# Optimization experiments

Hardware: AMD Instinct MI355X
Metric: run time of the kernel (lower is better)

Reference implementation:

```python
import jax, jax.numpy as jnp
import numpy as np

B, S, D, H, DH, M = 4, 4096, 1024, 16, 64, 128


def _create_projection_matrix(m, d, seed=0):
    # Block-orthogonal Gaussian projection (FAVOR+), same math as the numpy helper.
    np.random.seed(seed)
    n_block = m // d
    blocks = []
    for _ in range(n_block):
        block = np.random.normal(0, 1, (d, d))
        q, _ = np.linalg.qr(block)
        blocks.append(q.T)
    rem = m - n_block * d
    if rem > 0:
        block = np.random.normal(0, 1, (d, d))
        q, _ = np.linalg.qr(block)
        blocks.append(q.T[:rem])
    proj = np.vstack(blocks)
    multiplier = np.linalg.norm(np.random.normal(0, 1, (m, d)), axis=1)
    return (np.diag(multiplier) @ proj).astype(np.float32)


def setup_inputs() -> dict:
    key = jax.random.key(0)
    ks = jax.random.split(key, 8)
    lim_attn = np.sqrt(6.0 / (D + H * DH)).astype(np.float32)
    lim_out = np.sqrt(6.0 / (H * DH + D)).astype(np.float32)
    head_pos = np.linspace(0.0 + 1.0 / (2.0 * H), 1.0, H, endpoint=False, dtype=np.float32).reshape(1, 1, H, 1)
    return {
        "source_input": jax.random.normal(ks[0], (B, S, D), jnp.float32),
        "pos_ft": jax.random.normal(ks[1], (B, S, D), jnp.float32),
        "pos_ft_slopes": jax.random.normal(ks[2], (B, S, D), jnp.float32),
        "value_weight": jax.random.uniform(ks[3], (D, H, DH), jnp.float32, -lim_attn, lim_attn),
        "pos_ft_weight": jax.random.uniform(ks[4], (D, H, DH), jnp.float32, -lim_attn, lim_attn),
        "pos_ft_scale": jnp.ones((1, 1, H, 1), jnp.float32),
        "pos_ft_offsets": jnp.asarray(head_pos),
        "output_weight": jax.random.uniform(ks[5], (H * DH, D), jnp.float32, -lim_out, lim_out),
        "projection_matrix": jnp.asarray(_create_projection_matrix(M, DH, seed=1234)),
    }


def _fourier_features(x, projection_matrix):
    # x: [b, l, h, d] -> [b, l, h, 2m]
    d = x.shape[-1]
    m = projection_matrix.shape[0]
    data_normalizer = 1.0 / (float(d) ** 0.25)
    ratio = 1.0 / (float(m) ** 0.5)
    xd = jnp.einsum('blhd,md->blhm', data_normalizer * x, projection_matrix)
    xd = jnp.clip(xd, -10000.0, 10000.0)
    return jnp.concatenate([ratio * jnp.sin(xd), ratio * jnp.cos(xd)], axis=-1)


def reference(source_input, pos_ft, pos_ft_slopes, value_weight, pos_ft_weight,
              pos_ft_scale, pos_ft_offsets, output_weight, projection_matrix):
    # Projections
    value = jnp.einsum('bnm,mhd->bnhd', source_input, value_weight)        # [B,S,H,DH]
    pos_proj = jnp.einsum('bnm,mhd->bnhd', pos_ft, pos_ft_weight)          # [B,S,H,DH]
    slope_proj = jnp.einsum('bnm,mhd->bnhd', pos_ft_slopes, pos_ft_weight) # [B,S,H,DH]

    query_pos = pos_ft_scale * pos_proj
    key_pos = query_pos + pos_ft_offsets * (pos_ft_scale * slope_proj)

    # FAVOR fourier random features
    q_prime = _fourier_features(query_pos, projection_matrix)  # [B,S,H,2M]
    k_prime = _fourier_features(key_pos, projection_matrix)    # [B,S,H,2M]

    # Linear attention: O(L) kvs accumulation (non-causal, normalize_attn=False)
    kvs = jnp.einsum('blhm,blhd->bhmd', k_prime, value)         # [B,H,2M,DH]
    av = jnp.einsum('blhm,bhmd->blhd', q_prime, kvs)            # [B,S,H,DH]

    slen = av.shape[1]
    norms = jnp.linalg.norm(slope_proj, axis=-1, keepdims=True) / float(slen)
    av = norms * av

    out = jnp.einsum('bnm,md->bnd', av.reshape(av.shape[0], slen, -1), output_weight)
    # Dropout is identity at inference (training=False)
    return out
```

## Files before the change

### kernel.cpp

```cpp
#include <hip/hip_runtime.h>
#include <math.h>


typedef unsigned short u16;
typedef __attribute__((ext_vector_type(8))) short bf16x8;
typedef __attribute__((ext_vector_type(4))) float floatx4;

__device__ __forceinline__ float bf2f(u16 u) {
  union { unsigned int i; float f; } v; v.i = ((unsigned int)u) << 16; return v.f;
}
__device__ __forceinline__ u16 f2bf(float f) {
  union { float f; unsigned int i; } v; v.f = f;
  unsigned int r = v.i + 0x7fffu + ((v.i >> 16) & 1u);
  return (u16)(r >> 16);
}
__device__ __forceinline__ bool wire_f32(const unsigned* probe) {
  return probe[0] == 0x3F800000u;
}
__device__ __forceinline__ void gload_lds16(const void* g, void* l) {
  __builtin_amdgcn_global_load_lds(
      (const __attribute__((address_space(1))) void*)g,
      (__attribute__((address_space(3))) void*)l, 16, 0, 0);
}

__device__ __forceinline__ void gemm_body(
    const u16* __restrict__ A, int lda, const u16* __restrict__ B, int ldb,
    void* __restrict__ C, long coff, int Klog, int fold, int ofmt, bool f32w,
    long m0, long n0, u16* sA, u16* sB)
{
  const int t = threadIdx.x;
  const int wave = t >> 6, lane = t & 63;
  const int ll = lane & 15, quad = lane >> 4;
  const int wm0 = (wave >> 1) * 64, wn0 = (wave & 1) * 64;
  const int lr = lane >> 2, lc = (lane & 3) * 8;
  floatx4 acc[4][4];
  floatx4 zero = {0.0f, 0.0f, 0.0f, 0.0f};
  #pragma unroll
  for (int i = 0; i < 4; i++)
    #pragma unroll
    for (int j = 0; j < 4; j++) acc[i][j] = zero;

  for (int kc = 0; kc < Klog; kc += 32) {
    int akc = kc, bkc = kc;
    if (fold) {
      akc = (kc < 1024) ? kc : kc - 1024;
      bkc = (kc < 2048) ? kc : kc - 2048;
    }
    #pragma unroll
    for (int j = 0; j < 2; j++) {
      int r0 = wave * 32 + j * 16;
      gload_lds16(&A[(m0 + r0 + lr) * (long)lda + akc + lc], &sA[r0 * 32]);
      gload_lds16(&B[(n0 + r0 + lr) * (long)ldb + bkc + lc], &sB[r0 * 32]);
    }
    __syncthreads();
    bf16x8 af[4], bfr[4];
    #pragma unroll
    for (int i = 0; i < 4; i++) {
      af[i]  = *(const bf16x8*)&sA[(wm0 + i * 16 + ll) * 32 + quad * 8];
      bfr[i] = *(const bf16x8*)&sB[(wn0 + i * 16 + ll) * 32 + quad * 8];
    }
    #pragma unroll
    for (int i = 0; i < 4; i++)
      #pragma unroll
      for (int j = 0; j < 4; j++)
        acc[i][j] = __builtin_amdgcn_mfma_f32_16x16x32_bf16(af[i], bfr[j], acc[i][j], 0, 0, 0);
    __syncthreads();
  }
  #pragma unroll
  for (int i = 0; i < 4; i++)
    #pragma unroll
    for (int j = 0; j < 4; j++)
      #pragma unroll
      for (int r = 0; r < 4; r++) {
        long row = m0 + wm0 + i * 16 + quad * 4 + r;
        long col = n0 + wn0 + j * 16 + ll;
        float v = acc[i][j][r];
        long addr = coff + row * 1024 + col;
        if (ofmt == 0) ((u16*)C)[addr] = f2bf(v);
        else if (ofmt == 1) ((float*)C)[addr] = v;
        else if (f32w) ((float*)C)[addr] = v;
        else ((u16*)C)[addr] = f2bf(v);
      }
}

__global__ __launch_bounds__(256) void gemm_gl(
    const u16* __restrict__ A, int lda, const u16* __restrict__ B, int ldb,
    void* __restrict__ C, long coff, int Klog, int fold, int ofmt,
    const unsigned* __restrict__ probe)
{
  __shared__ u16 sA[128 * 32], sB[128 * 32];
  gemm_body(A, lda, B, ldb, C, coff, Klog, fold, ofmt, wire_f32(probe),
            (long)blockIdx.x * 128, (long)blockIdx.y * 128, sA, sB);
}

__global__ __launch_bounds__(256) void gemm_mega(
    const u16* __restrict__ A2, const u16* __restrict__ W2,
    float* __restrict__ posp, const u16* __restrict__ srcb,
    const u16* __restrict__ wvt, u16* __restrict__ valb,
    const unsigned* __restrict__ probe)
{
  __shared__ u16 sA[128 * 32], sB[128 * 32];
  const bool f32w = wire_f32(probe);
  int id = blockIdx.x;
  if (id < 512) {
    gemm_body(A2, 2048, W2, 2048, posp, 0, 3072, 1, 1, f32w,
              (long)(id >> 3) * 128, (long)(id & 7) * 128, sA, sB);
  } else {
    int v = id - 512;
    gemm_body(srcb, 1024, wvt, 1024, valb, 0, 1024, 0, 0, f32w,
              (long)(v >> 3) * 128, (long)(v & 7) * 128, sA, sB);
  }
}

__device__ __forceinline__ void split_body(
    const void* __restrict__ Aw, long aoff, u16* __restrict__ A2, int rowbase,
    bool f32w, long idx)
{
  int row = (int)(idx >> 7);
  int c8 = (int)(idx & 127) * 8;
  u16 h8[8], l8[8];
  if (f32w) {
    const float* ap = (const float*)Aw + aoff + (long)row * 1024 + c8;
    #pragma unroll
    for (int e = 0; e < 8; e++) {
      float v = ap[e]; u16 hb = f2bf(v);
      h8[e] = hb; l8[e] = f2bf(v - bf2f(hb));
    }
  } else {
    *(uint4*)h8 = *(const uint4*)((const u16*)Aw + aoff + (long)row * 1024 + c8);
    #pragma unroll
    for (int e = 0; e < 8; e++) l8[e] = 0;
  }
  u16* orow = A2 + (long)(rowbase + row) * 2048;
  *(uint4*)&orow[c8] = *(uint4*)h8;
  *(uint4*)&orow[1024 + c8] = *(uint4*)l8;
}

__device__ __forceinline__ void conv_body(
    const void* __restrict__ Aw, long aoff, u16* __restrict__ out,
    bool f32w, long idx)
{
  long base = idx * 8;
  u16 h8[8];
  if (f32w) {
    const float* ap = (const float*)Aw + aoff + base;
    #pragma unroll
    for (int e = 0; e < 8; e++) h8[e] = f2bf(ap[e]);
  } else {
    *(uint4*)h8 = *(const uint4*)((const u16*)Aw + aoff + base);
  }
  *(uint4*)&out[base] = *(uint4*)h8;
}

__global__ __launch_bounds__(256) void split_hilo(
    const void* __restrict__ Aw, long aoff, u16* __restrict__ A2, int rowbase,
    const unsigned* __restrict__ probe)
{
  split_body(Aw, aoff, A2, rowbase, wire_f32(probe),
             (long)blockIdx.x * 256 + threadIdx.x);
}

__global__ __launch_bounds__(256) void conv_bf16(
    const void* __restrict__ Aw, long aoff, u16* __restrict__ out,
    const unsigned* __restrict__ probe)
{
  conv_body(Aw, aoff, out, wire_f32(probe),
            (long)blockIdx.x * 256 + threadIdx.x);
}

__global__ __launch_bounds__(256) void mega2(
    const u16* __restrict__ av, const u16* __restrict__ wot,
    void* __restrict__ dout, long coff,
    const void* __restrict__ posf, const void* __restrict__ slpf,
    const void* __restrict__ src, long ioff_next,
    u16* __restrict__ A2, u16* __restrict__ srcb,
    const unsigned* __restrict__ probe)
{
  __shared__ u16 sA[128 * 32], sB[128 * 32];
  const bool f32w = wire_f32(probe);
  int id = blockIdx.x;
  if (id < 256) {
    gemm_body(av, 1024, wot, 1024, dout, coff, 1024, 0, 2, f32w,
              (long)(id >> 3) * 128, (long)(id & 7) * 128, sA, sB);
  } else if (id < 2304) {
    split_body(posf, ioff_next, A2, 0, f32w,
               (long)(id - 256) * 256 + threadIdx.x);
  } else if (id < 4352) {
    split_body(slpf, ioff_next, A2, 4096, f32w,
               (long)(id - 2304) * 256 + threadIdx.x);
  } else {
    conv_body(src, ioff_next, srcb, f32w,
              (long)(id - 4352) * 256 + threadIdx.x);
  }
}

__global__ __launch_bounds__(256) void transpose_w(
    const void* __restrict__ in, u16* __restrict__ outb,
    const unsigned* __restrict__ probe)
{
  __shared__ float s[64][65];
  const bool f32w = wire_f32(probe);
  int t = threadIdx.x;
  int r0 = blockIdx.y * 64, c0 = blockIdx.x * 64;
  for (int u = t; u < 4096; u += 256) {
    int r = u >> 6, c = u & 63;
    long idx = (long)(r0 + r) * 1024 + c0 + c;
    s[c][r] = f32w ? ((const float*)in)[idx] : bf2f(((const u16*)in)[idx]);
  }
  __syncthreads();
  for (int u = t; u < 4096; u += 256) {
    int r = u >> 6, c = u & 63;
    outb[(long)(c0 + r) * 1024 + r0 + c] = f2bf(s[r][c]);
  }
}

__global__ __launch_bounds__(256) void transpose_w2(
    const void* __restrict__ in, u16* __restrict__ out2,
    const unsigned* __restrict__ probe)
{
  __shared__ float s[64][65];
  const bool f32w = wire_f32(probe);
  int t = threadIdx.x;
  int r0 = blockIdx.y * 64, c0 = blockIdx.x * 64;
  for (int u = t; u < 4096; u += 256) {
    int r = u >> 6, c = u & 63;
    long idx = (long)(r0 + r) * 1024 + c0 + c;
    s[c][r] = f32w ? ((const float*)in)[idx] : bf2f(((const u16*)in)[idx]);
  }
  __syncthreads();
  for (int u = t; u < 4096; u += 256) {
    int r = u >> 6, c = u & 63;
    float v = s[r][c];
    u16 hb = f2bf(v);
    long rowb = (long)(c0 + r) * 2048;
    out2[rowb + r0 + c] = hb;
    out2[rowb + 1024 + r0 + c] = f2bf(v - bf2f(hb));
  }
}

__global__ __launch_bounds__(256) void proj_prep(
    const void* __restrict__ proj, u16* __restrict__ P2,
    const unsigned* __restrict__ probe)
{
  const bool f32w = wire_f32(probe);
  int idx = blockIdx.x * 256 + threadIdx.x;
  int m = idx >> 6, d = idx & 63;
  const float dn = 0.3535533905932738f;
  float v = dn * (f32w ? ((const float*)proj)[idx] : bf2f(((const u16*)proj)[idx]));
  u16 hb = f2bf(v);
  P2[(long)m * 128 + d] = hb;
  P2[(long)m * 128 + 64 + d] = f2bf(v - bf2f(hb));
}

__global__ __launch_bounds__(256) void featurize_mfma(
    const float* __restrict__ posp, const float* __restrict__ slpp,
    const u16* __restrict__ P2, const void* __restrict__ scl,
    const void* __restrict__ offs, u16* __restrict__ qp, u16* __restrict__ kpT,
    const unsigned* __restrict__ probe, int h0)
{
  __shared__ u16 sAp[4 * 64 * 32], sAs[4 * 64 * 32], sB[4 * 128 * 32];
  const bool f32w = wire_f32(probe);
  const int t = threadIdx.x;
  const int wave = t >> 6, lane = t & 63;
  const int ll = lane & 15, quad = lane >> 4;
  const int wm0 = (wave >> 1) * 32, wn0 = (wave & 1) * 64;
  const int g = blockIdx.y, h = h0 + g;
  const int l0 = blockIdx.x * 64;
  const float s1 = f32w ? ((const float*)scl)[h] : bf2f(((const u16*)scl)[h]);
  const float s2 = (f32w ? ((const float*)offs)[h] : bf2f(((const u16*)offs)[h])) * s1;
  const float ratio = 0.08838834764831845f;

  for (int u = t; u < 512; u += 256) {
    int r = u >> 3, cc = u & 7;
    const float* pp = posp + (long)(l0 + r) * 1024 + h * 64 + cc * 8;
    const float* sp = slpp + (long)(l0 + r) * 1024 + h * 64 + cc * 8;
    u16 ph[8], pl[8], sh[8], sl[8];
    #pragma unroll
    for (int e = 0; e < 8; e++) {
      float vp = pp[e]; u16 hb = f2bf(vp);
      ph[e] = hb; pl[e] = f2bf(vp - bf2f(hb));
      float vs = sp[e]; u16 sb = f2bf(vs);
      sh[e] = sb; sl[e] = f2bf(vs - bf2f(sb));
    }
    int ch = cc >> 2, cw = (cc & 3) * 8;
    *(uint4*)&sAp[((ch) * 64 + r) * 32 + cw]     = *(uint4*)ph;
    *(uint4*)&sAp[((2 + ch) * 64 + r) * 32 + cw] = *(uint4*)pl;
    *(uint4*)&sAs[((ch) * 64 + r) * 32 + cw]     = *(uint4*)sh;
    *(uint4*)&sAs[((2 + ch) * 64 + r) * 32 + cw] = *(uint4*)sl;
  }
  for (int u = t; u < 2048; u += 256) {
    int r = u >> 4, q4 = u & 15;
    uint4 v = *(const uint4*)&P2[(long)r * 128 + q4 * 8];
    int ch = q4 >> 2, cw = (q4 & 3) * 8;
    *(uint4*)&sB[(ch * 128 + r) * 32 + cw] = v;
  }
  __syncthreads();

  floatx4 accp[2][4], accs[2][4];
  floatx4 zero = {0.0f, 0.0f, 0.0f, 0.0f};
  #pragma unroll
  for (int i = 0; i < 2; i++)
    #pragma unroll
    for (int j = 0; j < 4; j++) { accp[i][j] = zero; accs[i][j] = zero; }

  const int ACH[6] = {0, 1, 0, 1, 2, 3};
  const int BCH[6] = {0, 1, 2, 3, 0, 1};
  #pragma unroll
  for (int kci = 0; kci < 6; kci++) {
    int ac = ACH[kci], bc = BCH[kci];
    bf16x8 ap[2], as2[2], bfr[4];
    #pragma unroll
    for (int i = 0; i < 2; i++) {
      ap[i]  = *(const bf16x8*)&sAp[(ac * 64 + wm0 + i * 16 + ll) * 32 + quad * 8];
      as2[i] = *(const bf16x8*)&sAs[(ac * 64 + wm0 + i * 16 + ll) * 32 + quad * 8];
    }
    #pragma unroll
    for (int j = 0; j < 4; j++)
      bfr[j] = *(const bf16x8*)&sB[(bc * 128 + wn0 + j * 16 + ll) * 32 + quad * 8];
    #pragma unroll
    for (int i = 0; i < 2; i++)
      #pragma unroll
      for (int j = 0; j < 4; j++) {
        accp[i][j] = __builtin_amdgcn_mfma_f32_16x16x32_bf16(ap[i],  bfr[j], accp[i][j], 0, 0, 0);
        accs[i][j] = __builtin_amdgcn_mfma_f32_16x16x32_bf16(as2[i], bfr[j], accs[i][j], 0, 0, 0);
      }
  }

  #pragma unroll
  for (int i = 0; i < 2; i++) {
    int lbase = l0 + wm0 + i * 16 + quad * 4;
    #pragma unroll
    for (int j = 0; j < 4; j++) {
      int m = wn0 + j * 16 + ll;
      u16 ksin[4], kcos[4];
      #pragma unroll
      for (int r = 0; r < 4; r++) {
        float dq = s1 * accp[i][j][r];
        float dk = dq + s2 * accs[i][j][r];
        dq = fminf(fmaxf(dq, -10000.0f), 10000.0f);
        dk = fminf(fmaxf(dk, -10000.0f), 10000.0f);
        long qbase = ((long)g * 4096 + lbase + r) * 256;
        qp[qbase + m]       = f2bf(ratio * __sinf(dq));
        qp[qbase + m + 128] = f2bf(ratio * __cosf(dq));
        ksin[r] = f2bf(ratio * __sinf(dk));
        kcos[r] = f2bf(ratio * __cosf(dk));
      }
      *(uint2*)&kpT[((long)(g * 256 + m)) * 4096 + lbase]       = *(uint2*)ksin;
      *(uint2*)&kpT[((long)(g * 256 + m + 128)) * 4096 + lbase] = *(uint2*)kcos;
    }
  }
}

__global__ __launch_bounds__(256) void transpose_v(
    const u16* __restrict__ in, u16* __restrict__ out)
{
  __shared__ u16 s[64][72];
  int t = threadIdx.x;
  int c0 = blockIdx.x * 64;
  int r0 = blockIdx.y * 64;
  for (int u = t; u < 512; u += 256) {
    int r = u >> 3, c8 = (u & 7) * 8;
    uint4 v = *(const uint4*)&in[(long)(r0 + r) * 1024 + c0 + c8];
    const u16* pv = (const u16*)&v;
    #pragma unroll
    for (int e = 0; e < 8; e++) s[c8 + e][r] = pv[e];
  }
  __syncthreads();
  for (int u = t; u < 512; u += 256) {
    int r = u >> 3, c8 = (u & 7) * 8;
    *(uint4*)&out[(long)(c0 + r) * 4096 + r0 + c8] = *(const uint4*)&s[r][c8];
  }
}

__global__ __launch_bounds__(256) void norm_kernel(
    const float* __restrict__ slp, float* __restrict__ nrm)
{
  int idx = blockIdx.x * 256 + threadIdx.x;
  int row = idx >> 4, h = idx & 15;
  const float* p = slp + (long)row * 1024 + h * 64;
  float acc = 0.0f;
  #pragma unroll
  for (int i = 0; i < 16; i++) {
    float4 v = *(const float4*)&p[i * 4];
    acc += v.x * v.x + v.y * v.y + v.z * v.z + v.w * v.w;
  }
  nrm[idx] = sqrtf(acc) * (1.0f / 4096.0f);
}

__global__ __launch_bounds__(256) void kvs_mfma(
    const u16* __restrict__ kpT, const u16* __restrict__ vT,
    float* __restrict__ kvp, int h0)
{
  __shared__ u16 sA[256][40], sB[64][40];
  const int t = threadIdx.x;
  const int wave = t >> 6, lane = t & 63;
  const int ll = lane & 15, quad = lane >> 4;
  const int wm0 = wave * 64;
  const int ks = blockIdx.x, g = blockIdx.y;
  const int G = gridDim.y, KS = gridDim.x;
  const int h = h0 + g;
  const int lch = 4096 / KS;
  const int lbase = ks * lch;
  floatx4 acc[4][4];
  floatx4 zero = {0.0f, 0.0f, 0.0f, 0.0f};
  #pragma unroll
  for (int i = 0; i < 4; i++)
    #pragma unroll
    for (int j = 0; j < 4; j++) acc[i][j] = zero;

  for (int kc = 0; kc < lch; kc += 32) {
    for (int u = t; u < 1024; u += 256) {
      int r = u >> 2, s = u & 3;
      *(uint4*)&sA[r][s * 8] =
          *(const uint4*)&kpT[((long)(g * 256 + r)) * 4096 + lbase + kc + s * 8];
    }
    {
      int r = t >> 2, s = t & 3;
      if (t < 256)
        *(uint4*)&sB[r][s * 8] =
            *(const uint4*)&vT[((long)(h * 64 + r)) * 4096 + lbase + kc + s * 8];
    }
    __syncthreads();
    bf16x8 af[4], bfr[4];
    #pragma unroll
    for (int i = 0; i < 4; i++) {
      af[i] = *(const bf16x8*)&sA[wm0 + i * 16 + ll][quad * 8];
      bfr[i] = *(const bf16x8*)&sB[i * 16 + ll][quad * 8];
    }
    #pragma unroll
    for (int i = 0; i < 4; i++)
      #pragma unroll
      for (int j = 0; j < 4; j++)
        acc[i][j] = __builtin_amdgcn_mfma_f32_16x16x32_bf16(af[i], bfr[j], acc[i][j], 0, 0, 0);
    __syncthreads();
  }
  long obase = ((long)ks * G + g) * 256;
  #pragma unroll
  for (int i = 0; i < 4; i++)
    #pragma unroll
    for (int j = 0; j < 4; j++)
      #pragma unroll
      for (int r = 0; r < 4; r++) {
        int row = wm0 + i * 16 + quad * 4 + r;
        int col = j * 16 + ll;
        kvp[(obase + row) * 64 + col] = acc[i][j][r];
      }
}

__global__ __launch_bounds__(256) void kvs_reduce(
    const float* __restrict__ kvp, u16* __restrict__ kvsTh,
    u16* __restrict__ kvsTl, int G, int KS)
{
  int idx = blockIdx.x * 256 + threadIdx.x;
  int m = idx & 255, d = (idx >> 8) & 63, g = idx >> 14;
  float s = 0.0f;
  for (int p = 0; p < KS; p++)
    s += kvp[(((long)p * G + g) * 256 + m) * 64 + d];
  u16 hb = f2bf(s);
  long o = ((long)g * 64 + d) * 256 + m;
  kvsTh[o] = hb;
  kvsTl[o] = f2bf(s - bf2f(hb));
}

__global__ __launch_bounds__(256) void av_mfma(
    const u16* __restrict__ qp, const u16* __restrict__ kvsTh,
    const u16* __restrict__ kvsTl, const float* __restrict__ nrm,
    u16* __restrict__ av, int h0)
{
  __shared__ u16 sA[128][40], sBh[64][40], sBl[64][40];
  const int t = threadIdx.x;
  const int wave = t >> 6, lane = t & 63;
  const int ll = lane & 15, quad = lane >> 4;
  const int wm0 = wave * 32;
  const int g = blockIdx.y, h = h0 + g;
  const int l0 = blockIdx.x * 128;
  floatx4 acc[2][4];
  floatx4 zero = {0.0f, 0.0f, 0.0f, 0.0f};
  #pragma unroll
  for (int i = 0; i < 2; i++)
    #pragma unroll
    for (int j = 0; j < 4; j++) acc[i][j] = zero;

  for (int kc = 0; kc < 256; kc += 32) {
    for (int u = t; u < 512; u += 256) {
      int r = u >> 2, s = u & 3;
      *(uint4*)&sA[r][s * 8] =
          *(const uint4*)&qp[((long)g * 4096 + l0 + r) * 256 + kc + s * 8];
    }
    {
      int r = t >> 2, s4 = t & 3;
      long o = ((long)g * 64 + r) * 256 + kc + s4 * 8;
      *(uint4*)&sBh[r][s4 * 8] = *(const uint4*)&kvsTh[o];
      *(uint4*)&sBl[r][s4 * 8] = *(const uint4*)&kvsTl[o];
    }
    __syncthreads();
    bf16x8 af[2], bh[4], bl[4];
    #pragma unroll
    for (int i = 0; i < 2; i++)
      af[i] = *(const bf16x8*)&sA[wm0 + i * 16 + ll][quad * 8];
    #pragma unroll
    for (int j = 0; j < 4; j++) {
      bh[j] = *(const bf16x8*)&sBh[j * 16 + ll][quad * 8];
      bl[j] = *(const bf16x8*)&sBl[j * 16 + ll][quad * 8];
    }
    #pragma unroll
    for (int i = 0; i < 2; i++)
      #pragma unroll
      for (int j = 0; j < 4; j++) {
        acc[i][j] = __builtin_amdgcn_mfma_f32_16x16x32_bf16(af[i], bh[j], acc[i][j], 0, 0, 0);
        acc[i][j] = __builtin_amdgcn_mfma_f32_16x16x32_bf16(af[i], bl[j], acc[i][j], 0, 0, 0);
      }
    __syncthreads();
  }
  #pragma unroll
  for (int i = 0; i < 2; i++)
    #pragma unroll
    for (int r = 0; r < 4; r++) {
      int l = l0 + wm0 + i * 16 + quad * 4 + r;
      float nv = nrm[l * 16 + h];
      #pragma unroll
      for (int j = 0; j < 4; j++) {
        int d = j * 16 + ll;
        av[(long)l * 1024 + h * 64 + d] = f2bf(acc[i][j][r] * nv);
      }
    }
}

extern "C" void kernel_launch(void* const* d_in, const int* in_sizes, int n_in,
                              void* d_out, int out_size, void* d_ws, size_t ws_size,
                              hipStream_t stream) {
  const void* src  = d_in[0];
  const void* posf = d_in[1];
  const void* slpf = d_in[2];
  const void* wv   = d_in[3];
  const void* wp   = d_in[4];
  const void* scl  = d_in[5];
  const void* offs = d_in[6];
  const void* wo   = d_in[7];
  const void* proj = d_in[8];
  const unsigned* probe = (const unsigned*)d_in[5];
  char* ws = (char*)d_ws;
  const size_t KiB = 1024;
  const size_t MiB = 1024 * 1024;

  u16*   wvt   = (u16*)(ws + 0 * MiB);
  u16*   wot   = (u16*)(ws + 2 * MiB);
  u16*   W2    = (u16*)(ws + 4 * MiB);
  float* nrm   = (float*)(ws + 8 * MiB);
  u16*   P2    = (u16*)(ws + 8 * MiB + 256 * KiB);
  u16*   kvsTh = (u16*)(ws + 8 * MiB + 320 * KiB);
  u16*   kvsTl = (u16*)(ws + 8 * MiB + 832 * KiB);
  float* posp  = (float*)(ws + 10 * MiB);
  float* slpp  = (float*)(ws + 26 * MiB);
  u16*   valb  = (u16*)(ws + 42 * MiB);
  u16*   av    = valb;
  u16*   vT    = (u16*)(ws + 50 * MiB);
  char*  dyn   = ws + 58 * MiB;

  const int KS = 16;
  int G = 1;
  int stacked = 0;
  if (ws_size >= 122 * MiB) { G = 16; stacked = 1; }
  else if (ws_size >= 92 * MiB) { G = 4; stacked = 1; }
  u16* qp  = (u16*)dyn;
  u16* kpT = (u16*)(dyn + 2 * (size_t)G * MiB);
  u16* A2  = (u16*)dyn;
  u16* srcb = (G == 16) ? kpT : (u16*)dyn;
  float* kvp = (G == 16) ? posp : (float*)(dyn + 4 * (size_t)G * MiB);

  dim3 blk(256);
  transpose_w<<<dim3(16, 16), blk, 0, stream>>>(wv, wvt, probe);
  transpose_w<<<dim3(16, 16), blk, 0, stream>>>(wo, wot, probe);
  transpose_w2<<<dim3(16, 16), blk, 0, stream>>>(wp, W2, probe);
  proj_prep<<<dim3(32), blk, 0, stream>>>(proj, P2, probe);

  if (G == 16) {
    split_hilo<<<dim3(2048), blk, 0, stream>>>(posf, 0, A2, 0, probe);
    split_hilo<<<dim3(2048), blk, 0, stream>>>(slpf, 0, A2, 4096, probe);
    conv_bf16<<<dim3(2048), blk, 0, stream>>>(src, 0, srcb, probe);
    for (int b = 0; b < 4; b++) {
      long ioff = (long)b * 4096 * 1024;
      gemm_mega<<<dim3(768), blk, 0, stream>>>(A2, W2, posp, srcb, wvt, valb, probe);
      norm_kernel<<<dim3(256), blk, 0, stream>>>(slpp, nrm);
      transpose_v<<<dim3(16, 64), blk, 0, stream>>>(valb, vT);
      featurize_mfma<<<dim3(64, 16), blk, 0, stream>>>(
          posp, slpp, P2, scl, offs, qp, kpT, probe, 0);
      kvs_mfma<<<dim3(KS, 16), blk, 0, stream>>>(kpT, vT, kvp, 0);
      kvs_reduce<<<dim3(16 * 64), blk, 0, stream>>>(kvp, kvsTh, kvsTl, 16, KS);
      av_mfma<<<dim3(32, 16), blk, 0, stream>>>(qp, kvsTh, kvsTl, nrm, av, 0);
      if (b < 3) {
        long ioff_n = (long)(b + 1) * 4096 * 1024;
        mega2<<<dim3(6400), blk, 0, stream>>>(av, wot, d_out, ioff,
                                              posf, slpf, src, ioff_n,
                                              A2, srcb, probe);
      } else {
        gemm_gl<<<dim3(32, 8), blk, 0, stream>>>(av, 1024, wot, 1024,
                                                 d_out, ioff, 1024, 0, 2, probe);
      }
    }
  } else {
    for (int b = 0; b < 4; b++) {
      long ioff = (long)b * 4096 * 1024;
      if (stacked) {
        split_hilo<<<dim3(2048), blk, 0, stream>>>(posf, ioff, A2, 0, probe);
        split_hilo<<<dim3(2048), blk, 0, stream>>>(slpf, ioff, A2, 4096, probe);
        gemm_gl<<<dim3(64, 8), blk, 0, stream>>>(A2, 2048, W2, 2048,
                                                 posp, 0, 3072, 1, 1, probe);
      } else {
        split_hilo<<<dim3(2048), blk, 0, stream>>>(posf, ioff, A2, 0, probe);
        gemm_gl<<<dim3(32, 8), blk, 0, stream>>>(A2, 2048, W2, 2048,
                                                 posp, 0, 3072, 1, 1, probe);
        split_hilo<<<dim3(2048), blk, 0, stream>>>(slpf, ioff, A2, 0, probe);
        gemm_gl<<<dim3(32, 8), blk, 0, stream>>>(A2, 2048, W2, 2048,
                                                 slpp, 0, 3072, 1, 1, probe);
      }
      norm_kernel<<<dim3(256), blk, 0, stream>>>(slpp, nrm);
      conv_bf16<<<dim3(2048), blk, 0, stream>>>(src, ioff, srcb, probe);
      gemm_gl<<<dim3(32, 8), blk, 0, stream>>>(srcb, 1024, wvt, 1024,
                                               valb, 0, 1024, 0, 0, probe);
      transpose_v<<<dim3(16, 64), blk, 0, stream>>>(valb, vT);
      for (int hg = 0; hg < 16; hg += G) {
        featurize_mfma<<<dim3(64, G), blk, 0, stream>>>(
            posp, slpp, P2, scl, offs, qp, kpT, probe, hg);
        kvs_mfma<<<dim3(KS, G), blk, 0, stream>>>(kpT, vT, kvp, hg);
        kvs_reduce<<<dim3(G * 64), blk, 0, stream>>>(kvp, kvsTh, kvsTl, G, KS);
        av_mfma<<<dim3(32, G), blk, 0, stream>>>(qp, kvsTh, kvsTl, nrm, av, hg);
      }
      gemm_gl<<<dim3(32, 8), blk, 0, stream>>>(av, 1024, wot, 1024,
                                               d_out, ioff, 1024, 0, 2, probe);
    }
  }
}
```

Baseline: 1.116 ms.

## Specialize gemm_mega with split-bf16 MFMA, fused value transpose, and XCD-aware tile mapping

Replaces the generic gemm_body calls in gemm_mega with inlined specialized paths. The position GEMM now loads hi and lo halves of both operands per K step and issues three MFMAs (hi*hi, hi*lo, lo*hi), instead of walking a folded K of 3072. The value GEMM writes its bf16 output transposed through LDS straight into vT, so the separate transpose_v launch and the valb round trip are gone. Block-to-tile mappings in gemm_mega and mega2 are permuted so that blocks on the same XCD share row and column tiles for L2 reuse, at the cost of more LDS use and register pressure.

```diff
diff --git a/kernel.cpp b/kernel.cpp
--- a/kernel.cpp
+++ b/kernel.cpp
@@ -96,19 +96,108 @@
 __global__ __launch_bounds__(256) void gemm_mega(
     const u16* __restrict__ A2, const u16* __restrict__ W2,
     float* __restrict__ posp, const u16* __restrict__ srcb,
-    const u16* __restrict__ wvt, u16* __restrict__ valb,
+    const u16* __restrict__ wvt, u16* __restrict__ vT,
     const unsigned* __restrict__ probe)
 {
-  __shared__ u16 sA[128 * 32], sB[128 * 32];
-  const bool f32w = wire_f32(probe);
-  int id = blockIdx.x;
-  if (id < 512) {
-    gemm_body(A2, 2048, W2, 2048, posp, 0, 3072, 1, 1, f32w,
-              (long)(id >> 3) * 128, (long)(id & 7) * 128, sA, sB);
+  __shared__ u16 pool[20480];
+  const int id = blockIdx.x;
+  const int xcd = id & 7, pos = id >> 3;
+  const int t = threadIdx.x;
+  const int wave = t >> 6, lane = t & 63;
+  const int ll = lane & 15, quad = lane >> 4;
+  const int wm0 = (wave >> 1) * 64, wn0 = (wave & 1) * 64;
+  const int lr = lane >> 2, lc = (lane & 3) * 8;
+  floatx4 acc[4][4];
+  floatx4 zero = {0.0f, 0.0f, 0.0f, 0.0f};
+  #pragma unroll
+  for (int i = 0; i < 4; i++)
+    #pragma unroll
+    for (int j = 0; j < 4; j++) acc[i][j] = zero;
+
+  if (pos < 64) {
+    int tile = xcd * 64 + pos;
+    long m0 = (long)(tile >> 3) * 128, n0 = (long)(tile & 7) * 128;
+    u16* sAh = pool;
+    u16* sAl = pool + 4096;
+    u16* sBh = pool + 8192;
+    u16* sBl = pool + 12288;
+    for (int kc = 0; kc < 1024; kc += 32) {
+      #pragma unroll
+      for (int j = 0; j < 2; j++) {
+        int r0 = wave * 32 + j * 16;
+        gload_lds16(&A2[(m0 + r0 + lr) * 2048 + kc + lc],        &sAh[r0 * 32]);
+        gload_lds16(&A2[(m0 + r0 + lr) * 2048 + 1024 + kc + lc], &sAl[r0 * 32]);
+        gload_lds16(&W2[(n0 + r0 + lr) * 2048 + kc + lc],        &sBh[r0 * 32]);
+        gload_lds16(&W2[(n0 + r0 + lr) * 2048 + 1024 + kc + lc], &sBl[r0 * 32]);
+      }
+      __syncthreads();
+      bf16x8 ah[4], al[4], bh[4], bl[4];
+      #pragma unroll
+      for (int i = 0; i < 4; i++) {
+        ah[i] = *(const bf16x8*)&sAh[(wm0 + i * 16 + ll) * 32 + quad * 8];
+        al[i] = *(const bf16x8*)&sAl[(wm0 + i * 16 + ll) * 32 + quad * 8];
+        bh[i] = *(const bf16x8*)&sBh[(wn0 + i * 16 + ll) * 32 + quad * 8];
+        bl[i] = *(const bf16x8*)&sBl[(wn0 + i * 16 + ll) * 32 + quad * 8];
+      }
+      #pragma unroll
+      for (int i = 0; i < 4; i++)
+        #pragma unroll
+        for (int j = 0; j < 4; j++) {
+          acc[i][j] = __builtin_amdgcn_mfma_f32_16x16x32_bf16(ah[i], bh[j], acc[i][j], 0, 0, 0);
+          acc[i][j] = __builtin_amdgcn_mfma_f32_16x16x32_bf16(ah[i], bl[j], acc[i][j], 0, 0, 0);
+          acc[i][j] = __builtin_amdgcn_mfma_f32_16x16x32_bf16(al[i], bh[j], acc[i][j], 0, 0, 0);
+        }
+      __syncthreads();
+    }
+    #pragma unroll
+    for (int i = 0; i < 4; i++)
+      #pragma unroll
+      for (int j = 0; j < 4; j++)
+        #pragma unroll
+        for (int r = 0; r < 4; r++) {
+          long row = m0 + wm0 + i * 16 + quad * 4 + r;
+          long col = n0 + wn0 + j * 16 + ll;
+          posp[row * 1024 + col] = acc[i][j][r];
+        }
   } else {
-    int v = id - 512;
-    gemm_body(srcb, 1024, wvt, 1024, valb, 0, 1024, 0, 0, f32w,
-              (long)(v >> 3) * 128, (long)(v & 7) * 128, sA, sB);
+    int v = xcd * 32 + (pos - 64);
+    long m0 = (long)(v >> 3) * 128, n0 = (long)(v & 7) * 128;
+    u16* sA = pool;
+    u16* sB = pool + 4096;
+    for (int kc = 0; kc < 1024; kc += 32) {
+      #pragma unroll
+      for (int j = 0; j < 2; j++) {
+        int r0 = wave * 32 + j * 16;
+        gload_lds16(&srcb[(m0 + r0 + lr) * 1024 + kc + lc], &sA[r0 * 32]);
+        gload_lds16(&wvt[(n0 + r0 + lr) * 1024 + kc + lc],  &sB[r0 * 32]);
+      }
+      __syncthreads();
+      bf16x8 af[4], bfr[4];
+      #pragma unroll
+      for (int i = 0; i < 4; i++) {
+        af[i]  = *(const bf16x8*)&sA[(wm0 + i * 16 + ll) * 32 + quad * 8];
+        bfr[i] = *(const bf16x8*)&sB[(wn0 + i * 16 + ll) * 32 + quad * 8];
+      }
+      #pragma unroll
+      for (int i = 0; i < 4; i++)
+        #pragma unroll
+        for (int j = 0; j < 4; j++)
+          acc[i][j] = __builtin_amdgcn_mfma_f32_16x16x32_bf16(af[i], bfr[j], acc[i][j], 0, 0, 0);
+      __syncthreads();
+    }
+    u16 (*sT)[136] = (u16(*)[136])pool;
+    #pragma unroll
+    for (int i = 0; i < 4; i++)
+      #pragma unroll
+      for (int j = 0; j < 4; j++)
+        #pragma unroll
+        for (int r = 0; r < 4; r++)
+          sT[wn0 + j * 16 + ll][wm0 + i * 16 + quad * 4 + r] = f2bf(acc[i][j][r]);
+    __syncthreads();
+    for (int u = t; u < 2048; u += 256) {
+      int d = u >> 4, c8 = (u & 15) * 8;
+      *(uint4*)&vT[(n0 + d) * 4096 + m0 + c8] = *(const uint4*)&sT[d][c8];
+    }
   }
 }
 
@@ -180,8 +269,9 @@
   const bool f32w = wire_f32(probe);
   int id = blockIdx.x;
   if (id < 256) {
+    int tile = (id & 7) * 32 + (id >> 3);
     gemm_body(av, 1024, wot, 1024, dout, coff, 1024, 0, 2, f32w,
-              (long)(id >> 3) * 128, (long)(id & 7) * 128, sA, sB);
+              (long)(tile >> 3) * 128, (long)(tile & 7) * 128, sA, sB);
   } else if (id < 2304) {
     split_body(posf, ioff_next, A2, 0, f32w,
                (long)(id - 256) * 256 + threadIdx.x);
@@ -580,9 +670,8 @@
     conv_bf16<<<dim3(2048), blk, 0, stream>>>(src, 0, srcb, probe);
     for (int b = 0; b < 4; b++) {
       long ioff = (long)b * 4096 * 1024;
-      gemm_mega<<<dim3(768), blk, 0, stream>>>(A2, W2, posp, srcb, wvt, valb, probe);
+      gemm_mega<<<dim3(768), blk, 0, stream>>>(A2, W2, posp, srcb, wvt, vT, probe);
       norm_kernel<<<dim3(256), blk, 0, stream>>>(slpp, nrm);
-      transpose_v<<<dim3(16, 64), blk, 0, stream>>>(valb, vT);
       featurize_mfma<<<dim3(64, 16), blk, 0, stream>>>(
           posp, slpp, P2, scl, offs, qp, kpT, probe, 0);
       kvs_mfma<<<dim3(KS, 16), blk, 0, stream>>>(kpT, vT, kvp, 0);
```

After: 936.4 us. -16.1%, faster.
